# Performance work log

Measured on AMD Instinct MI355X. Metric: run time of the kernel, lower is better.

Reference implementation:

```python
import jax, jax.numpy as jnp
import numpy as np

E, K = 16, 4
D, H = 1024, 1024
B, M = 64, 16
OUT = 10


def setup_inputs() -> dict:
    key = jax.random.key(0)
    ks = jax.random.split(key, 8)
    s = 0.02  # weight init scale
    return {
        "mm_embed": jax.random.normal(ks[0], (B, M, D), jnp.float32),
        "w_gate": jax.random.normal(ks[1], (D, E), jnp.float32) * s,
        "W1": jax.random.normal(ks[2], (E, D, H), jnp.float32) * s,
        "b1": jnp.zeros((E, H), jnp.float32),
        "W2": jax.random.normal(ks[3], (E, H, D), jnp.float32) * s,
        "b2": jnp.zeros((E, D), jnp.float32),
        "ln_w": jnp.ones((D,), jnp.float32),
        "ln_b": jnp.zeros((D,), jnp.float32),
        "W_los": jax.random.normal(ks[4], (D, OUT), jnp.float32) * s,
        "b_los": jnp.zeros((OUT,), jnp.float32),
        "true_y": jax.random.uniform(ks[5], (B, OUT), jnp.float32),
        "task_index": 3,
    }


def _cv_squared(v):
    eps = 1e-10
    v = v.astype(jnp.float32)
    return jnp.var(v, ddof=1) / (jnp.mean(v) ** 2 + eps)  # torch .var() is unbiased


def reference(mm_embed, w_gate, W1, b1, W2, b2, ln_w, ln_b, W_los, b_los, true_y, task_index):
    b, m, d = mm_embed.shape
    x = mm_embed.reshape(-1, d)                       # [N, D] tokens
    n = x.shape[0]

    # ---- top-k gating (eval mode: clean logits, no noise) ----
    logits = x @ w_gate                               # [N, E]
    top_logits, top_idx = jax.lax.top_k(logits, K + 1)
    tk_logits = top_logits[:, :K]                     # [N, K]
    tk_idx = top_idx[:, :K]
    tk_gates = jax.nn.softmax(tk_logits, axis=1)
    gates = jnp.zeros((n, E), x.dtype).at[jnp.arange(n)[:, None], tk_idx].set(tk_gates)

    importance = gates.sum(0)                         # [E]
    load = (gates > 0).sum(0)                         # [E] (eval-mode load)
    loss = (_cv_squared(importance) + _cv_squared(load)) * 0.01

    # ---- expert MLPs + gated combine (math-equivalent to sparse dispatch) ----
    h = jax.nn.relu(jnp.einsum('nd,edh->enh', x, W1) + b1[:, None, :])   # [E, N, H]
    o = jnp.einsum('enh,eho->eno', h, W2) + b2[:, None, :]               # [E, N, D]
    y = jnp.einsum('ne,eno->no', gates, o)                               # [N, D]

    # ---- combine over modalities + LayerNorm ----
    mm_moe = y.reshape(b, m, d).sum(axis=1)           # [B, D]
    mu = jnp.mean(mm_moe, axis=-1, keepdims=True)
    var = jnp.var(mm_moe, axis=-1, keepdims=True)
    final = (mm_moe - mu) / jnp.sqrt(var + 1e-5) * ln_w + ln_b

    scores = final @ W_los + b_los                    # [B, 10]
    pred_loss = jnp.mean((scores - true_y) ** 2)      # MSE criterion
    return (scores, loss, pred_loss)
```

## Files before the change

### kernel.cpp

```cpp
#include <hip/hip_runtime.h>
#include <hip/hip_bf16.h>

#define D_DIM 1024
#define H_DIMN 1024
#define N_TOK 1024
#define N_EXP 16
#define TOPK  4
#define N_PAIR (N_TOK*TOPK)
#define B_SZ  64
#define OUT_SZ 10
#define MAX_TILES 48

typedef __attribute__((ext_vector_type(8))) short short8_t;
typedef __attribute__((ext_vector_type(4))) float f32x4;

static constexpr size_t WS_TKIDX   = 0;
static constexpr size_t WS_TKGATE  = 16384;
static constexpr size_t WS_OFFSETS = 32768;
static constexpr size_t WS_TE      = 33024;
static constexpr size_t WS_TRS     = 33280;
static constexpr size_t WS_NTILE   = 33536;
static constexpr size_t WS_PERMTOK = 33792;
static constexpr size_t WS_PAIRROW = 50176;
static constexpr size_t WS_XS      = 131072;
static constexpr size_t WS_HS      = 4325376;
static constexpr size_t WS_OBUF    = 21102592;
static constexpr size_t WS_WT      = 37879808;

__device__ __forceinline__ unsigned short f2bf_rn(float f) {
  unsigned int u = __float_as_uint(f);
  unsigned int r = (u + 0x7fffu + ((u >> 16) & 1u)) >> 16;
  return (unsigned short)r;
}
__device__ __forceinline__ void splitf(float f, short& h, short& l) {
  unsigned short hu = f2bf_rn(f);
  float fh = __uint_as_float(((unsigned int)hu) << 16);
  unsigned short lu = f2bf_rn(f - fh);
  h = (short)hu; l = (short)lu;
}

__global__ __launch_bounds__(256) void split_w_kernel(
    const float* __restrict__ W, short* __restrict__ WT)
{
  __shared__ float tb[32][132];
  const int nt = blockIdx.x, kb = blockIdx.y, e = blockIdx.z;
  const int t = threadIdx.x;
  const float* src = W + ((size_t)e << 20) + (size_t)(kb * 32) * 1024 + nt * 128;
  const int rk = t >> 3;
  const int rc = (t & 7) * 16;
  #pragma unroll
  for (int j = 0; j < 4; j++)
    *(float4*)&tb[rk][rc + j*4] = *(const float4*)(src + (size_t)rk * 1024 + rc + j*4);
  __syncthreads();
  const int n  = t >> 1;
  const int kh = (t & 1) * 16;
  short h[16], l[16];
  #pragma unroll
  for (int i = 0; i < 16; i++) splitf(tb[kh + i][n], h[i], l[i]);
  short* dst = WT + (((size_t)e * 32 + kb) * 1024 + nt * 128 + n) * 64;
  *(short8_t*)(dst + kh)          = *(short8_t*)&h[0];
  *(short8_t*)(dst + kh + 8)      = *(short8_t*)&h[8];
  *(short8_t*)(dst + 32 + kh)     = *(short8_t*)&l[0];
  *(short8_t*)(dst + 32 + kh + 8) = *(short8_t*)&l[8];
}

__global__ __launch_bounds__(256) void gate_kernel(
    const float* __restrict__ x, const float* __restrict__ wg,
    int* __restrict__ tk_idx, float* __restrict__ tk_gates,
    short* __restrict__ xs)
{
  int wave = threadIdx.x >> 6, lane = threadIdx.x & 63;
  int n = blockIdx.x * 4 + wave;
  const float* xr = x + (size_t)n * D_DIM + lane * 16;
  float xv[16];
  #pragma unroll
  for (int j = 0; j < 4; j++) {
    float4 v = *(const float4*)(xr + j*4);
    xv[j*4+0] = v.x; xv[j*4+1] = v.y; xv[j*4+2] = v.z; xv[j*4+3] = v.w;
  }

  {
    short h[16], l[16];
    #pragma unroll
    for (int i = 0; i < 16; i++) splitf(xv[i], h[i], l[i]);
    short* base = xs + (size_t)n * 2048 + (lane >> 1) * 64 + (lane & 1) * 16;
    *(short8_t*)(base)          = *(short8_t*)&h[0];
    *(short8_t*)(base + 8)      = *(short8_t*)&h[8];
    *(short8_t*)(base + 32)     = *(short8_t*)&l[0];
    *(short8_t*)(base + 32 + 8) = *(short8_t*)&l[8];
  }

  float lg[N_EXP];
  #pragma unroll
  for (int e = 0; e < N_EXP; e++) lg[e] = 0.f;
  #pragma unroll
  for (int i = 0; i < 16; i++) {
    float xvi = xv[i];
    const float4* wrow = (const float4*)(wg + (size_t)(lane * 16 + i) * N_EXP);
    float4 w0 = wrow[0], w1 = wrow[1], w2 = wrow[2], w3 = wrow[3];
    lg[0]  = fmaf(xvi, w0.x, lg[0]);  lg[1]  = fmaf(xvi, w0.y, lg[1]);
    lg[2]  = fmaf(xvi, w0.z, lg[2]);  lg[3]  = fmaf(xvi, w0.w, lg[3]);
    lg[4]  = fmaf(xvi, w1.x, lg[4]);  lg[5]  = fmaf(xvi, w1.y, lg[5]);
    lg[6]  = fmaf(xvi, w1.z, lg[6]);  lg[7]  = fmaf(xvi, w1.w, lg[7]);
    lg[8]  = fmaf(xvi, w2.x, lg[8]);  lg[9]  = fmaf(xvi, w2.y, lg[9]);
    lg[10] = fmaf(xvi, w2.z, lg[10]); lg[11] = fmaf(xvi, w2.w, lg[11]);
    lg[12] = fmaf(xvi, w3.x, lg[12]); lg[13] = fmaf(xvi, w3.y, lg[13]);
    lg[14] = fmaf(xvi, w3.z, lg[14]); lg[15] = fmaf(xvi, w3.w, lg[15]);
  }
  #pragma unroll
  for (int e = 0; e < N_EXP; e++) {
    float s = lg[e];
    #pragma unroll
    for (int off = 32; off; off >>= 1) s += __shfl_xor(s, off);
    lg[e] = s;
  }

  float tv[TOPK]; int ti[TOPK];
  #pragma unroll
  for (int k = 0; k < TOPK; k++) {
    float mv = -3.4e38f; int mi = 0;
    #pragma unroll
    for (int e = 0; e < N_EXP; e++) if (lg[e] > mv) { mv = lg[e]; mi = e; }
    tv[k] = mv; ti[k] = mi; lg[mi] = -3.4e38f;
  }
  float mx = tv[0];
  float ex[TOPK]; float ssum = 0.f;
  #pragma unroll
  for (int k = 0; k < TOPK; k++) { ex[k] = expf(tv[k] - mx); ssum += ex[k]; }
  float inv = 1.f / ssum;

  if (lane < TOPK) {
    tk_idx  [n*TOPK + lane] = ti[lane];
    tk_gates[n*TOPK + lane] = ex[lane] * inv;
  }
}

__global__ __launch_bounds__(1024) void scan_scatter_kernel(
    const int* __restrict__ tk_idx, const float* __restrict__ tk_gates,
    int* __restrict__ offsets, int* __restrict__ perm_tok, int* __restrict__ pair_row,
    int* __restrict__ te, int* __restrict__ trs, int* __restrict__ ntile,
    float* __restrict__ out)
{
  __shared__ int cnt[N_EXP];
  __shared__ float fimp[N_EXP];
  __shared__ int cur[N_EXP];
  const int tid = threadIdx.x;
  if (tid < N_EXP) { cnt[tid] = 0; fimp[tid] = 0.f; }
  __syncthreads();
  #pragma unroll
  for (int pp = 0; pp < N_PAIR; pp += 1024) {
    int p = pp + tid;
    int e = tk_idx[p];
    atomicAdd(&cnt[e], 1);
    atomicAdd(&fimp[e], tk_gates[p]);
  }
  __syncthreads();
  if (tid == 0) {
    int off = 0;
    for (int e = 0; e < N_EXP; e++) { offsets[e] = off; cur[e] = off; off += cnt[e]; }
    offsets[N_EXP] = off;
    float mi = 0.f, ml = 0.f;
    for (int e = 0; e < N_EXP; e++) { mi += fimp[e]; ml += (float)cnt[e]; }
    mi *= (1.f/N_EXP); ml *= (1.f/N_EXP);
    float vi = 0.f, vl = 0.f;
    for (int e = 0; e < N_EXP; e++) {
      float di = fimp[e] - mi;          vi += di*di;
      float dl = (float)cnt[e] - ml;    vl += dl*dl;
    }
    vi *= (1.f/(N_EXP-1)); vl *= (1.f/(N_EXP-1));
    out[640] = 0.01f * (vi/(mi*mi + 1e-10f) + vl/(ml*ml + 1e-10f));
    out[641] = 0.f;
    int T = 0;
    for (int e = 0; e < N_EXP; e++) {
      int nt = (cnt[e] + 127) >> 7;
      for (int s = 0; s < nt; s++) { te[T] = e; trs[T] = offsets[e] + s*128; T++; }
    }
    *ntile = T;
  }
  __syncthreads();
  #pragma unroll
  for (int pp = 0; pp < N_PAIR; pp += 1024) {
    int p = pp + tid;
    int row = atomicAdd(&cur[tk_idx[p]], 1);
    perm_tok[row] = p >> 2;
    pair_row[p] = row;
  }
}

template<int GATHER, int RELU, int SPLITOUT>
__global__ __launch_bounds__(256) void ffn_gemm(
    const short* __restrict__ As,
    const short* __restrict__ WT,
    const float* __restrict__ bias,
    float* __restrict__ OutF,
    short* __restrict__ OutS,
    const int* __restrict__ offsets,
    const int* __restrict__ perm_tok,
    const int* __restrict__ te, const int* __restrict__ trs,
    const int* __restrict__ ntile)
{
  __shared__ short Ah[128][40], Al[128][40], Bh[128][40], Bl[128][40];

  const int ti = blockIdx.x;
  if (ti >= *ntile) return;
  const int e = te[ti];
  const int row_start = trs[ti];
  const int rows_here = min(128, offsets[e+1] - row_start);
  const int colbase = blockIdx.y * 128;
  const int tid = threadIdx.x;

  const int srow = tid >> 1;
  const int ssel = tid & 1;
  int arow_g = row_start + min(srow, rows_here - 1);
  if (GATHER) arow_g = perm_tok[arow_g];
  const short* a_ptr = As + (size_t)arow_g * 2048 + ssel * 32;
  const short* b_ptr = WT + (size_t)e * 2097152 + (size_t)(colbase + srow) * 64 + ssel * 32;

  short* aw = ssel ? &Al[srow][0] : &Ah[srow][0];
  short* bw = ssel ? &Bl[srow][0] : &Bh[srow][0];
  const int rotW = (srow >> 3) & 3;

  const int lane = tid & 63;
  const int wid  = tid >> 6;
  const int wr = wid >> 1, wc = wid & 1;
  const int l16 = lane & 15, l4 = lane >> 4;
  const int ar0 = wr * 64 + l16;
  const int br0 = wc * 64 + l16;

  int aoff[4], boff[4];
  #pragma unroll
  for (int m = 0; m < 4; m++) {
    int R = ar0 + m * 16;
    aoff[m] = R * 40 + ((l4 + (R >> 3)) & 3) * 8;
    int S = br0 + m * 16;
    boff[m] = S * 40 + ((l4 + (S >> 3)) & 3) * 8;
  }
  const short* Ah0 = &Ah[0][0]; const short* Al0 = &Al[0][0];
  const short* Bh0 = &Bh[0][0]; const short* Bl0 = &Bl[0][0];

  f32x4 acc[4][4];
  #pragma unroll
  for (int i = 0; i < 4; i++)
    #pragma unroll
    for (int j = 0; j < 4; j++) acc[i][j] = (f32x4)(0.f);

  short8_t rA[4], rB[4];
  #pragma unroll
  for (int j = 0; j < 4; j++) {
    rA[j] = *(const short8_t*)(a_ptr + j * 8);
    rB[j] = *(const short8_t*)(b_ptr + j * 8);
  }

  for (int t = 0; t < 32; t++) {
    #pragma unroll
    for (int j = 0; j < 4; j++) {
      *(short8_t*)(aw + ((j + rotW) & 3) * 8) = rA[j];
      *(short8_t*)(bw + ((j + rotW) & 3) * 8) = rB[j];
    }
    __syncthreads();

    if (t < 31) {
      const short* ap = a_ptr + (t + 1) * 64;
      const short* bp = b_ptr + (size_t)(t + 1) * 65536;
      #pragma unroll
      for (int j = 0; j < 4; j++) {
        rA[j] = *(const short8_t*)(ap + j * 8);
        rB[j] = *(const short8_t*)(bp + j * 8);
      }
    }

    short8_t AH[4], AL[4], BH[4], BL[4];
    #pragma unroll
    for (int m = 0; m < 4; m++) {
      AH[m] = *(const short8_t*)(Ah0 + aoff[m]);
      AL[m] = *(const short8_t*)(Al0 + aoff[m]);
      BH[m] = *(const short8_t*)(Bh0 + boff[m]);
      BL[m] = *(const short8_t*)(Bl0 + boff[m]);
    }
    #pragma unroll
    for (int n = 0; n < 4; n++)
      #pragma unroll
      for (int m = 0; m < 4; m++)
        acc[m][n] = __builtin_amdgcn_mfma_f32_16x16x32_bf16(AH[m], BH[n], acc[m][n], 0, 0, 0);
    #pragma unroll
    for (int n = 0; n < 4; n++)
      #pragma unroll
      for (int m = 0; m < 4; m++)
        acc[m][n] = __builtin_amdgcn_mfma_f32_16x16x32_bf16(AH[m], BL[n], acc[m][n], 0, 0, 0);
    #pragma unroll
    for (int n = 0; n < 4; n++)
      #pragma unroll
      for (int m = 0; m < 4; m++)
        acc[m][n] = __builtin_amdgcn_mfma_f32_16x16x32_bf16(AL[m], BH[n], acc[m][n], 0, 0, 0);
    __syncthreads();
  }

  float bvals[4];
  #pragma unroll
  for (int n = 0; n < 4; n++)
    bvals[n] = bias[e * H_DIMN + colbase + wc*64 + n*16 + l16];

  #pragma unroll
  for (int m = 0; m < 4; m++) {
    #pragma unroll
    for (int n = 0; n < 4; n++) {
      const int col = colbase + wc*64 + n*16 + l16;
      #pragma unroll
      for (int j = 0; j < 4; j++) {
        int lr = wr*64 + m*16 + l4*4 + j;
        if (lr < rows_here) {
          float v = acc[m][n][j] + bvals[n];
          if (RELU) v = fmaxf(v, 0.f);
          size_t row = (size_t)(row_start + lr);
          if (SPLITOUT) {
            short hs, ls; splitf(v, hs, ls);
            size_t idx = row * 2048 + (col >> 5) * 64 + (col & 31);
            OutS[idx]      = hs;
            OutS[idx + 32] = ls;
          } else {
            OutF[row * H_DIMN + col] = v;
          }
        }
      }
    }
  }
}

__global__ __launch_bounds__(256) void moe_ln_kernel(
    const float* __restrict__ O,
    const float* __restrict__ tk_gates,
    const int* __restrict__ pair_row,
    const float* __restrict__ ln_w, const float* __restrict__ ln_b,
    const float* __restrict__ W_los, const float* __restrict__ b_los,
    const float* __restrict__ true_y,
    float* __restrict__ out)
{
  __shared__ float fin[D_DIM];
  __shared__ float redx[256];
  __shared__ float redy[256];
  const int b = blockIdx.x, tid = threadIdx.x;
  float4 acc = make_float4(0.f,0.f,0.f,0.f);
  for (int m = 0; m < 16; m++) {
    int n = b*16 + m;
    #pragma unroll
    for (int k = 0; k < TOPK; k++) {
      int p = n*TOPK + k;
      float g = tk_gates[p];
      int row = pair_row[p];
      float4 v = *(const float4*)&O[(size_t)row*D_DIM + tid*4];
      acc.x = fmaf(g, v.x, acc.x);
      acc.y = fmaf(g, v.y, acc.y);
      acc.z = fmaf(g, v.z, acc.z);
      acc.w = fmaf(g, v.w, acc.w);
    }
  }
  float s  = acc.x + acc.y + acc.z + acc.w;
  float s2 = acc.x*acc.x + acc.y*acc.y + acc.z*acc.z + acc.w*acc.w;
  redx[tid] = s; redy[tid] = s2;
  __syncthreads();
  for (int off = 128; off > 0; off >>= 1) {
    if (tid < off) { redx[tid] += redx[tid+off]; redy[tid] += redy[tid+off]; }
    __syncthreads();
  }
  float mean = redx[0] * (1.f/D_DIM);
  float var  = redy[0] * (1.f/D_DIM) - mean*mean;
  float rstd = rsqrtf(var + 1e-5f);

  int d0 = tid*4;
  fin[d0+0] = (acc.x - mean)*rstd*ln_w[d0+0] + ln_b[d0+0];
  fin[d0+1] = (acc.y - mean)*rstd*ln_w[d0+1] + ln_b[d0+1];
  fin[d0+2] = (acc.z - mean)*rstd*ln_w[d0+2] + ln_b[d0+2];
  fin[d0+3] = (acc.w - mean)*rstd*ln_w[d0+3] + ln_b[d0+3];
  __syncthreads();

  const int wv = tid >> 6, ln = tid & 63;
  for (int o = wv; o < OUT_SZ; o += 4) {
    float p = 0.f;
    for (int d = ln; d < D_DIM; d += 64) p = fmaf(fin[d], W_los[d*OUT_SZ + o], p);
    #pragma unroll
    for (int off = 32; off; off >>= 1) p += __shfl_xor(p, off);
    if (ln == 0) {
      float sc = p + b_los[o];
      out[b*OUT_SZ + o] = sc;
      float d = sc - true_y[b*OUT_SZ + o];
      atomicAdd(&out[641], d * d * (1.f/(B_SZ*OUT_SZ)));
    }
  }
}

extern "C" void kernel_launch(void* const* d_in, const int* in_sizes, int n_in,
                              void* d_out, int out_size, void* d_ws, size_t ws_size,
                              hipStream_t stream) {
  const float* x      = (const float*)d_in[0];
  const float* wg     = (const float*)d_in[1];
  const float* W1     = (const float*)d_in[2];
  const float* b1     = (const float*)d_in[3];
  const float* W2     = (const float*)d_in[4];
  const float* b2     = (const float*)d_in[5];
  const float* ln_w   = (const float*)d_in[6];
  const float* ln_b   = (const float*)d_in[7];
  const float* W_los  = (const float*)d_in[8];
  const float* b_los  = (const float*)d_in[9];
  const float* true_y = (const float*)d_in[10];
  float* out = (float*)d_out;
  char* ws = (char*)d_ws;

  int*   tk_idx   = (int*)  (ws + WS_TKIDX);
  float* tk_gates = (float*)(ws + WS_TKGATE);
  int*   offsets  = (int*)  (ws + WS_OFFSETS);
  int*   te       = (int*)  (ws + WS_TE);
  int*   trs      = (int*)  (ws + WS_TRS);
  int*   ntile    = (int*)  (ws + WS_NTILE);
  int*   perm_tok = (int*)  (ws + WS_PERMTOK);
  int*   pair_row = (int*)  (ws + WS_PAIRROW);
  short* xs       = (short*)(ws + WS_XS);
  short* Hs       = (short*)(ws + WS_HS);
  float* Obuf     = (float*)(ws + WS_OBUF);
  short* WT       = (short*)(ws + WS_WT);

  split_w_kernel<<<dim3(8, 32, 16), 256, 0, stream>>>(W1, WT);
  gate_kernel<<<256, 256, 0, stream>>>(x, wg, tk_idx, tk_gates, xs);
  scan_scatter_kernel<<<1, 1024, 0, stream>>>(tk_idx, tk_gates, offsets,
                                              perm_tok, pair_row, te, trs, ntile, out);
  ffn_gemm<1,1,1><<<dim3(MAX_TILES, 8), 256, 0, stream>>>(
      xs, WT, b1, nullptr, Hs, offsets, perm_tok, te, trs, ntile);
  split_w_kernel<<<dim3(8, 32, 16), 256, 0, stream>>>(W2, WT);
  ffn_gemm<0,0,0><<<dim3(MAX_TILES, 8), 256, 0, stream>>>(
      Hs, WT, b2, Obuf, nullptr, offsets, perm_tok, te, trs, ntile);
  moe_ln_kernel<<<64, 256, 0, stream>>>(Obuf, tk_gates, pair_row, ln_w, ln_b,
                                        W_los, b_los, true_y, out);
}
```

Baseline: 362.0 us.

## Pre-swizzle weights into MFMA fragment layout and load A fragments directly from global

The weight split kernel now writes bf16 hi/lo weights in a layout that matches the MFMA operand fragments. The GEMM can then copy B tiles into double-buffered LDS without swizzling, and it reads A fragments straight from global memory into registers, which removes the A staging in LDS. The W1 split is merged with the gating kernel into a single prep launch, and the GEMM grid is flattened with launch_bounds(256,2) to allow higher occupancy. This raises register pressure and gives up coalesced A loads in exchange for fewer LDS round trips and barriers.

```diff
diff --git a/kernel.cpp b/kernel.cpp
--- a/kernel.cpp
+++ b/kernel.cpp
@@ -2,11 +2,9 @@
 #include <hip/hip_bf16.h>
 
 #define D_DIM 1024
-#define H_DIMN 1024
-#define N_TOK 1024
 #define N_EXP 16
 #define TOPK  4
-#define N_PAIR (N_TOK*TOPK)
+#define N_PAIR 4096
 #define B_SZ  64
 #define OUT_SZ 10
 #define MAX_TILES 48
@@ -39,46 +37,58 @@
   h = (short)hu; l = (short)lu;
 }
 
+__device__ void split_job(const float* __restrict__ W, short* __restrict__ WT, int j) {
+  __shared__ float tb[32][132];
+  const int e = j >> 8, kb = (j >> 3) & 31, cb = j & 7;
+  const int t = threadIdx.x;
+  const float* src = W + ((size_t)e << 20) + (size_t)(kb * 32) * 1024 + cb * 128;
+  {
+    const int rk = t >> 3, rc = (t & 7) * 16;
+    #pragma unroll
+    for (int q = 0; q < 4; q++)
+      *(float4*)&tb[rk][rc + q*4] = *(const float4*)(src + (size_t)rk * 1024 + rc + q*4);
+  }
+  __syncthreads();
+  short* dst = WT + (((size_t)e * 32 + kb) * 8 + cb) * 8192;
+  #pragma unroll
+  for (int q = 0; q < 2; q++) {
+    int ent = t + 256 * q;
+    int n = ent >> 6, l = ent & 63;
+    int l16 = l & 15, l4 = l >> 4;
+    short8_t hv, lv;
+    #pragma unroll
+    for (int i = 0; i < 8; i++) {
+      short hs, ls; splitf(tb[l4*8 + i][n*16 + l16], hs, ls);
+      hv[i] = hs; lv[i] = ls;
+    }
+    *(short8_t*)(dst + (n*2 + 0) * 512 + l*8) = hv;
+    *(short8_t*)(dst + (n*2 + 1) * 512 + l*8) = lv;
+  }
+}
+
 __global__ __launch_bounds__(256) void split_w_kernel(
-    const float* __restrict__ W, short* __restrict__ WT)
-{
-  __shared__ float tb[32][132];
-  const int nt = blockIdx.x, kb = blockIdx.y, e = blockIdx.z;
-  const int t = threadIdx.x;
-  const float* src = W + ((size_t)e << 20) + (size_t)(kb * 32) * 1024 + nt * 128;
-  const int rk = t >> 3;
-  const int rc = (t & 7) * 16;
-  #pragma unroll
-  for (int j = 0; j < 4; j++)
-    *(float4*)&tb[rk][rc + j*4] = *(const float4*)(src + (size_t)rk * 1024 + rc + j*4);
-  __syncthreads();
-  const int n  = t >> 1;
-  const int kh = (t & 1) * 16;
-  short h[16], l[16];
-  #pragma unroll
-  for (int i = 0; i < 16; i++) splitf(tb[kh + i][n], h[i], l[i]);
-  short* dst = WT + (((size_t)e * 32 + kb) * 1024 + nt * 128 + n) * 64;
-  *(short8_t*)(dst + kh)          = *(short8_t*)&h[0];
-  *(short8_t*)(dst + kh + 8)      = *(short8_t*)&h[8];
-  *(short8_t*)(dst + 32 + kh)     = *(short8_t*)&l[0];
-  *(short8_t*)(dst + 32 + kh + 8) = *(short8_t*)&l[8];
-}
-
-__global__ __launch_bounds__(256) void gate_kernel(
+    const float* __restrict__ W, short* __restrict__ WT) {
+  split_job(W, WT, blockIdx.x);
+}
+
+__global__ __launch_bounds__(256) void prep_kernel(
     const float* __restrict__ x, const float* __restrict__ wg,
+    const float* __restrict__ W1, short* __restrict__ WT,
     int* __restrict__ tk_idx, float* __restrict__ tk_gates,
     short* __restrict__ xs)
 {
-  int wave = threadIdx.x >> 6, lane = threadIdx.x & 63;
-  int n = blockIdx.x * 4 + wave;
+  const int bid = blockIdx.x;
+  if (bid < 4096) { split_job(W1, WT, bid); return; }
+
+  const int wave = threadIdx.x >> 6, lane = threadIdx.x & 63;
+  const int n = (bid - 4096) * 4 + wave;
   const float* xr = x + (size_t)n * D_DIM + lane * 16;
   float xv[16];
   #pragma unroll
-  for (int j = 0; j < 4; j++) {
-    float4 v = *(const float4*)(xr + j*4);
-    xv[j*4+0] = v.x; xv[j*4+1] = v.y; xv[j*4+2] = v.z; xv[j*4+3] = v.w;
-  }
-
+  for (int q = 0; q < 4; q++) {
+    float4 v = *(const float4*)(xr + q*4);
+    xv[q*4+0] = v.x; xv[q*4+1] = v.y; xv[q*4+2] = v.z; xv[q*4+3] = v.w;
+  }
   {
     short h[16], l[16];
     #pragma unroll
@@ -89,7 +99,6 @@
     *(short8_t*)(base + 32)     = *(short8_t*)&l[0];
     *(short8_t*)(base + 32 + 8) = *(short8_t*)&l[8];
   }
-
   float lg[N_EXP];
   #pragma unroll
   for (int e = 0; e < N_EXP; e++) lg[e] = 0.f;
@@ -114,23 +123,20 @@
     for (int off = 32; off; off >>= 1) s += __shfl_xor(s, off);
     lg[e] = s;
   }
-
-  float tv[TOPK]; int ti[TOPK];
+  float tv[TOPK]; int ti_[TOPK];
   #pragma unroll
   for (int k = 0; k < TOPK; k++) {
     float mv = -3.4e38f; int mi = 0;
     #pragma unroll
     for (int e = 0; e < N_EXP; e++) if (lg[e] > mv) { mv = lg[e]; mi = e; }
-    tv[k] = mv; ti[k] = mi; lg[mi] = -3.4e38f;
-  }
-  float mx = tv[0];
-  float ex[TOPK]; float ssum = 0.f;
+    tv[k] = mv; ti_[k] = mi; lg[mi] = -3.4e38f;
+  }
+  float mx = tv[0], ssum = 0.f, ex[TOPK];
   #pragma unroll
   for (int k = 0; k < TOPK; k++) { ex[k] = expf(tv[k] - mx); ssum += ex[k]; }
   float inv = 1.f / ssum;
-
   if (lane < TOPK) {
-    tk_idx  [n*TOPK + lane] = ti[lane];
+    tk_idx  [n*TOPK + lane] = ti_[lane];
     tk_gates[n*TOPK + lane] = ex[lane] * inv;
   }
 }
@@ -150,9 +156,8 @@
   #pragma unroll
   for (int pp = 0; pp < N_PAIR; pp += 1024) {
     int p = pp + tid;
-    int e = tk_idx[p];
-    atomicAdd(&cnt[e], 1);
-    atomicAdd(&fimp[e], tk_gates[p]);
+    atomicAdd(&cnt[tk_idx[p]], 1);
+    atomicAdd(&fimp[tk_idx[p]], tk_gates[p]);
   }
   __syncthreads();
   if (tid == 0) {
@@ -187,138 +192,152 @@
   }
 }
 
-template<int GATHER, int RELU, int SPLITOUT>
-__global__ __launch_bounds__(256) void ffn_gemm(
-    const short* __restrict__ As,
-    const short* __restrict__ WT,
+template<int IS_G1>
+__global__ __launch_bounds__(256, 2) void ffn_gemm(
+    const short* __restrict__ Asrc, const short* __restrict__ WTb,
     const float* __restrict__ bias,
-    float* __restrict__ OutF,
-    short* __restrict__ OutS,
-    const int* __restrict__ offsets,
-    const int* __restrict__ perm_tok,
-    const int* __restrict__ te, const int* __restrict__ trs,
-    const int* __restrict__ ntile)
+    float* __restrict__ OutF, short* __restrict__ OutS,
+    const int* __restrict__ offsets, const int* __restrict__ te,
+    const int* __restrict__ trs, const int* __restrict__ ntile,
+    const int* __restrict__ perm_tok)
 {
-  __shared__ short Ah[128][40], Al[128][40], Bh[128][40], Bl[128][40];
-
-  const int ti = blockIdx.x;
+  __shared__ short ldsB[2][8192];
+  const int job = blockIdx.x;
+  const int ti = job >> 3, cb = job & 7;
   if (ti >= *ntile) return;
   const int e = te[ti];
   const int row_start = trs[ti];
   const int rows_here = min(128, offsets[e+1] - row_start);
-  const int colbase = blockIdx.y * 128;
   const int tid = threadIdx.x;
-
-  const int srow = tid >> 1;
-  const int ssel = tid & 1;
-  int arow_g = row_start + min(srow, rows_here - 1);
-  if (GATHER) arow_g = perm_tok[arow_g];
-  const short* a_ptr = As + (size_t)arow_g * 2048 + ssel * 32;
-  const short* b_ptr = WT + (size_t)e * 2097152 + (size_t)(colbase + srow) * 64 + ssel * 32;
-
-  short* aw = ssel ? &Al[srow][0] : &Ah[srow][0];
-  short* bw = ssel ? &Bl[srow][0] : &Bh[srow][0];
-  const int rotW = (srow >> 3) & 3;
-
-  const int lane = tid & 63;
-  const int wid  = tid >> 6;
+  const int lane = tid & 63, wid = tid >> 6;
   const int wr = wid >> 1, wc = wid & 1;
   const int l16 = lane & 15, l4 = lane >> 4;
-  const int ar0 = wr * 64 + l16;
-  const int br0 = wc * 64 + l16;
-
-  int aoff[4], boff[4];
+
+  const short* abase[4];
   #pragma unroll
   for (int m = 0; m < 4; m++) {
-    int R = ar0 + m * 16;
-    aoff[m] = R * 40 + ((l4 + (R >> 3)) & 3) * 8;
-    int S = br0 + m * 16;
-    boff[m] = S * 40 + ((l4 + (S >> 3)) & 3) * 8;
-  }
-  const short* Ah0 = &Ah[0][0]; const short* Al0 = &Al[0][0];
-  const short* Bh0 = &Bh[0][0]; const short* Bl0 = &Bl[0][0];
+    int r = min(row_start + wr*64 + m*16 + l16, N_PAIR - 1);
+    size_t ar = IS_G1 ? (size_t)perm_tok[r] : (size_t)r;
+    abase[m] = Asrc + ar * 2048 + l4 * 8;
+  }
+  const short* wjb = WTb + ((size_t)e * 256 + cb) * 8192;
+  const int sg = (wid * 4) * 512 + lane * 8;
 
   f32x4 acc[4][4];
   #pragma unroll
   for (int i = 0; i < 4; i++)
     #pragma unroll
-    for (int j = 0; j < 4; j++) acc[i][j] = (f32x4)(0.f);
-
-  short8_t rA[4], rB[4];
-  #pragma unroll
-  for (int j = 0; j < 4; j++) {
-    rA[j] = *(const short8_t*)(a_ptr + j * 8);
-    rB[j] = *(const short8_t*)(b_ptr + j * 8);
-  }
-
-  for (int t = 0; t < 32; t++) {
-    #pragma unroll
-    for (int j = 0; j < 4; j++) {
-      *(short8_t*)(aw + ((j + rotW) & 3) * 8) = rA[j];
-      *(short8_t*)(bw + ((j + rotW) & 3) * 8) = rB[j];
-    }
-    __syncthreads();
-
-    if (t < 31) {
-      const short* ap = a_ptr + (t + 1) * 64;
-      const short* bp = b_ptr + (size_t)(t + 1) * 65536;
+    for (int jj = 0; jj < 4; jj++) acc[i][jj] = (f32x4)(0.f);
+
+  short8_t AH0[4], AL0[4], AH1[4], AL1[4], rBa[4], rBb[4];
+
+  #pragma unroll
+  for (int q = 0; q < 4; q++) rBa[q] = *(const short8_t*)(wjb + sg + q*512);
+  #pragma unroll
+  for (int q = 0; q < 4; q++) rBb[q] = *(const short8_t*)(wjb + 65536 + sg + q*512);
+  #pragma unroll
+  for (int m = 0; m < 4; m++) {
+    AH0[m] = *(const short8_t*)(abase[m]);
+    AL0[m] = *(const short8_t*)(abase[m] + 32);
+    AH1[m] = *(const short8_t*)(abase[m] + 64);
+    AL1[m] = *(const short8_t*)(abase[m] + 96);
+  }
+  #pragma unroll
+  for (int q = 0; q < 4; q++) *(short8_t*)&ldsB[0][sg + q*512] = rBa[q];
+  asm volatile("s_waitcnt lgkmcnt(0)" ::: "memory");
+  __builtin_amdgcn_s_barrier();
+
+  #define DO_MFMA48(AH, AL, BH, BL)                                                    \
+    { _Pragma("unroll")                                                                \
+      for (int n = 0; n < 4; n++) { _Pragma("unroll")                                  \
+        for (int m = 0; m < 4; m++)                                                    \
+          acc[m][n] = __builtin_amdgcn_mfma_f32_16x16x32_bf16(AH[m], BH[n], acc[m][n], 0,0,0); } \
+      _Pragma("unroll")                                                                \
+      for (int n = 0; n < 4; n++) { _Pragma("unroll")                                  \
+        for (int m = 0; m < 4; m++)                                                    \
+          acc[m][n] = __builtin_amdgcn_mfma_f32_16x16x32_bf16(AH[m], BL[n], acc[m][n], 0,0,0); } \
+      _Pragma("unroll")                                                                \
+      for (int n = 0; n < 4; n++) { _Pragma("unroll")                                  \
+        for (int m = 0; m < 4; m++)                                                    \
+          acc[m][n] = __builtin_amdgcn_mfma_f32_16x16x32_bf16(AL[m], BH[n], acc[m][n], 0,0,0); } }
+
+  for (int kbb = 0; kbb < 32; kbb += 2) {
+    {
+      short8_t BH[4], BL[4];
       #pragma unroll
-      for (int j = 0; j < 4; j++) {
-        rA[j] = *(const short8_t*)(ap + j * 8);
-        rB[j] = *(const short8_t*)(bp + j * 8);
-      }
-    }
-
-    short8_t AH[4], AL[4], BH[4], BL[4];
-    #pragma unroll
-    for (int m = 0; m < 4; m++) {
-      AH[m] = *(const short8_t*)(Ah0 + aoff[m]);
-      AL[m] = *(const short8_t*)(Al0 + aoff[m]);
-      BH[m] = *(const short8_t*)(Bh0 + boff[m]);
-      BL[m] = *(const short8_t*)(Bl0 + boff[m]);
-    }
-    #pragma unroll
-    for (int n = 0; n < 4; n++)
+      for (int n = 0; n < 4; n++) {
+        BH[n] = *(const short8_t*)&ldsB[0][((wc*4+n)*2 + 0)*512 + lane*8];
+        BL[n] = *(const short8_t*)&ldsB[0][((wc*4+n)*2 + 1)*512 + lane*8];
+      }
+      if (kbb + 2 < 32) {
+        #pragma unroll
+        for (int q = 0; q < 4; q++)
+          rBa[q] = *(const short8_t*)(wjb + (size_t)(kbb+2)*65536 + sg + q*512);
+      }
+      DO_MFMA48(AH0, AL0, BH, BL);
       #pragma unroll
-      for (int m = 0; m < 4; m++)
-        acc[m][n] = __builtin_amdgcn_mfma_f32_16x16x32_bf16(AH[m], BH[n], acc[m][n], 0, 0, 0);
-    #pragma unroll
-    for (int n = 0; n < 4; n++)
+      for (int q = 0; q < 4; q++) *(short8_t*)&ldsB[1][sg + q*512] = rBb[q];
+      if (kbb + 2 < 32) {
+        #pragma unroll
+        for (int m = 0; m < 4; m++) {
+          AH0[m] = *(const short8_t*)(abase[m] + (kbb+2)*64);
+          AL0[m] = *(const short8_t*)(abase[m] + (kbb+2)*64 + 32);
+        }
+      }
+      asm volatile("s_waitcnt lgkmcnt(0)" ::: "memory");
+      __builtin_amdgcn_s_barrier();
+    }
+    {
+      short8_t BH[4], BL[4];
       #pragma unroll
-      for (int m = 0; m < 4; m++)
-        acc[m][n] = __builtin_amdgcn_mfma_f32_16x16x32_bf16(AH[m], BL[n], acc[m][n], 0, 0, 0);
-    #pragma unroll
-    for (int n = 0; n < 4; n++)
+      for (int n = 0; n < 4; n++) {
+        BH[n] = *(const short8_t*)&ldsB[1][((wc*4+n)*2 + 0)*512 + lane*8];
+        BL[n] = *(const short8_t*)&ldsB[1][((wc*4+n)*2 + 1)*512 + lane*8];
+      }
+      if (kbb + 3 < 32) {
+        #pragma unroll
+        for (int q = 0; q < 4; q++)
+          rBb[q] = *(const short8_t*)(wjb + (size_t)(kbb+3)*65536 + sg + q*512);
+      }
+      DO_MFMA48(AH1, AL1, BH, BL);
+      if (kbb + 2 < 32) {
+        #pragma unroll
+        for (int q = 0; q < 4; q++) *(short8_t*)&ldsB[0][sg + q*512] = rBa[q];
+      }
+      if (kbb + 3 < 32) {
+        #pragma unroll
+        for (int m = 0; m < 4; m++) {
+          AH1[m] = *(const short8_t*)(abase[m] + (kbb+3)*64);
+          AL1[m] = *(const short8_t*)(abase[m] + (kbb+3)*64 + 32);
+        }
+      }
+      asm volatile("s_waitcnt lgkmcnt(0)" ::: "memory");
+      __builtin_amdgcn_s_barrier();
+    }
+  }
+  #undef DO_MFMA48
+
+  float bv[4];
+  #pragma unroll
+  for (int n = 0; n < 4; n++)
+    bv[n] = bias[e * 1024 + cb*128 + wc*64 + n*16 + l16];
+  #pragma unroll
+  for (int m = 0; m < 4; m++) {
+    #pragma unroll
+    for (int n = 0; n < 4; n++) {
+      const int col = cb*128 + wc*64 + n*16 + l16;
       #pragma unroll
-      for (int m = 0; m < 4; m++)
-        acc[m][n] = __builtin_amdgcn_mfma_f32_16x16x32_bf16(AL[m], BH[n], acc[m][n], 0, 0, 0);
-    __syncthreads();
-  }
-
-  float bvals[4];
-  #pragma unroll
-  for (int n = 0; n < 4; n++)
-    bvals[n] = bias[e * H_DIMN + colbase + wc*64 + n*16 + l16];
-
-  #pragma unroll
-  for (int m = 0; m < 4; m++) {
-    #pragma unroll
-    for (int n = 0; n < 4; n++) {
-      const int col = colbase + wc*64 + n*16 + l16;
-      #pragma unroll
-      for (int j = 0; j < 4; j++) {
-        int lr = wr*64 + m*16 + l4*4 + j;
+      for (int jj = 0; jj < 4; jj++) {
+        int lr = wr*64 + m*16 + l4*4 + jj;
         if (lr < rows_here) {
-          float v = acc[m][n][j] + bvals[n];
-          if (RELU) v = fmaxf(v, 0.f);
-          size_t row = (size_t)(row_start + lr);
-          if (SPLITOUT) {
+          float v = acc[m][n][jj] + bv[n];
+          if (IS_G1) {
+            v = fmaxf(v, 0.f);
             short hs, ls; splitf(v, hs, ls);
-            size_t idx = row * 2048 + (col >> 5) * 64 + (col & 31);
-            OutS[idx]      = hs;
-            OutS[idx + 32] = ls;
+            size_t o = (size_t)(row_start + lr) * 2048 + (col >> 5) * 64 + (col & 31);
+            OutS[o] = hs; OutS[o + 32] = ls;
           } else {
-            OutF[row * H_DIMN + col] = v;
+            OutF[(size_t)(row_start + lr) * 1024 + col] = v;
           }
         }
       }
@@ -365,14 +384,12 @@
   float mean = redx[0] * (1.f/D_DIM);
   float var  = redy[0] * (1.f/D_DIM) - mean*mean;
   float rstd = rsqrtf(var + 1e-5f);
-
   int d0 = tid*4;
   fin[d0+0] = (acc.x - mean)*rstd*ln_w[d0+0] + ln_b[d0+0];
   fin[d0+1] = (acc.y - mean)*rstd*ln_w[d0+1] + ln_b[d0+1];
   fin[d0+2] = (acc.z - mean)*rstd*ln_w[d0+2] + ln_b[d0+2];
   fin[d0+3] = (acc.w - mean)*rstd*ln_w[d0+3] + ln_b[d0+3];
   __syncthreads();
-
   const int wv = tid >> 6, ln = tid & 63;
   for (int o = wv; o < OUT_SZ; o += 4) {
     float p = 0.f;
@@ -418,15 +435,14 @@
   float* Obuf     = (float*)(ws + WS_OBUF);
   short* WT       = (short*)(ws + WS_WT);
 
-  split_w_kernel<<<dim3(8, 32, 16), 256, 0, stream>>>(W1, WT);
-  gate_kernel<<<256, 256, 0, stream>>>(x, wg, tk_idx, tk_gates, xs);
+  prep_kernel<<<4352, 256, 0, stream>>>(x, wg, W1, WT, tk_idx, tk_gates, xs);
   scan_scatter_kernel<<<1, 1024, 0, stream>>>(tk_idx, tk_gates, offsets,
                                               perm_tok, pair_row, te, trs, ntile, out);
-  ffn_gemm<1,1,1><<<dim3(MAX_TILES, 8), 256, 0, stream>>>(
-      xs, WT, b1, nullptr, Hs, offsets, perm_tok, te, trs, ntile);
-  split_w_kernel<<<dim3(8, 32, 16), 256, 0, stream>>>(W2, WT);
-  ffn_gemm<0,0,0><<<dim3(MAX_TILES, 8), 256, 0, stream>>>(
-      Hs, WT, b2, Obuf, nullptr, offsets, perm_tok, te, trs, ntile);
+  ffn_gemm<1><<<MAX_TILES*8, 256, 0, stream>>>(
+      xs, WT, b1, nullptr, Hs, offsets, te, trs, ntile, perm_tok);
+  split_w_kernel<<<4096, 256, 0, stream>>>(W2, WT);
+  ffn_gemm<0><<<MAX_TILES*8, 256, 0, stream>>>(
+      Hs, WT, b2, Obuf, nullptr, offsets, te, trs, ntile, perm_tok);
   moe_ln_kernel<<<64, 256, 0, stream>>>(Obuf, tk_gates, pair_row, ln_w, ln_b,
                                         W_los, b_los, true_y, out);
 }
```

New measurement: 395.9 us. 1.09x slower.
